# Kernel tuning notes

Hardware: AMD Instinct MI355X
Metric: run time of the kernel (lower is better)

## Reference

```python
import jax, jax.numpy as jnp
import numpy as np
from jax import lax

SCORE_THRESHOLD = 0.01
NMS_THRESHOLD = 0.5
MAX_DETECTIONS = 100
PRE_NMS_TOPK = 512  # fixed-shape candidate pool per class (tf NMS is unbounded; 512 >> max_detections covers it)
NEG_INF = -jnp.inf


def setup_inputs() -> dict:
    key = jax.random.key(0)
    k1, k2, k3, k4, k5 = jax.random.split(key, 5)
    B, N, C = 32, 50000, 10
    # valid (x1,y1,x2,y2) boxes: random top-left + positive width/height
    xy = jax.random.uniform(k1, (B, N, 2), dtype=jnp.float32) * 500.0
    wh = jax.random.uniform(k2, (B, N, 2), dtype=jnp.float32) * 100.0 + 1.0
    boxes = jnp.concatenate([xy, xy + wh], axis=-1)
    classification = jax.random.uniform(k3, (B, N, C), dtype=jnp.float32)
    rotation = jax.random.normal(k4, (B, N, 3), dtype=jnp.float32)
    translation = jax.random.normal(k5, (B, N, 3), dtype=jnp.float32)
    return {"boxes": boxes, "classification": classification,
            "rotation": rotation, "translation": translation}


def _iou_matrix(b):  # b: (K,4) in (x1,y1,x2,y2)
    x1, y1, x2, y2 = b[:, 0], b[:, 1], b[:, 2], b[:, 3]
    area = (x2 - x1) * (y2 - y1)  # (K,)
    ix1 = jnp.maximum(x1[:, None], x1[None, :])
    iy1 = jnp.maximum(y1[:, None], y1[None, :])
    ix2 = jnp.minimum(x2[:, None], x2[None, :])
    iy2 = jnp.minimum(y2[:, None], y2[None, :])
    inter = jnp.maximum(ix2 - ix1, 0.0) * jnp.maximum(iy2 - iy1, 0.0)
    union = area[:, None] + area[None, :] - inter
    return jnp.where(union > 0.0, inter / union, 0.0)  # (K,K)


def _greedy_nms_keep(iou, valid):
    # iou: (K,K) for boxes already sorted by descending score; valid: (K,) bool
    K = iou.shape[0]
    def body(suppressed, xs):
        iou_row, valid_i, i = xs
        keep_i = valid_i & jnp.logical_not(suppressed[i])
        suppressed = jnp.where(keep_i, suppressed | (iou_row > NMS_THRESHOLD), suppressed)
        return suppressed, keep_i
    _, keep = lax.scan(body, jnp.zeros((K,), bool), (iou, valid, jnp.arange(K)))
    return keep


def _per_class(scores, boxes_i):
    # scores: (N,), boxes_i: (N,4) -> kept candidate scores (K,) (-inf where dropped) and anchor idx (K,)
    sc = jnp.where(scores > SCORE_THRESHOLD, scores, NEG_INF)
    vals, idx = lax.top_k(sc, PRE_NMS_TOPK)          # sorted desc
    valid = vals > SCORE_THRESHOLD                    # also false for -inf pads
    iou = _iou_matrix(boxes_i[idx])
    keep = _greedy_nms_keep(iou, valid)
    keep = keep & (jnp.cumsum(keep.astype(jnp.int32)) <= MAX_DETECTIONS)
    return jnp.where(keep, vals, NEG_INF), idx


def _per_image(boxes_i, cls_i, rot_i, trans_i):
    # boxes_i (N,4), cls_i (N,C), rot_i (N,3), trans_i (N,3)
    C = cls_i.shape[1]
    sc_ck, idx_ck = jax.vmap(_per_class, in_axes=(1, None))(cls_i, boxes_i)  # (C,K)
    labels_ck = jnp.broadcast_to(jnp.arange(C, dtype=jnp.int32)[:, None], sc_ck.shape)
    sc_flat = sc_ck.reshape(-1)
    idx_flat = idx_ck.reshape(-1)
    lab_flat = labels_ck.reshape(-1)
    top_scores, sel = lax.top_k(sc_flat, MAX_DETECTIONS)   # global top-k across classes
    sel_idx = idx_flat[sel]
    sel_lab = lab_flat[sel]
    valid = jnp.isfinite(top_scores)
    out_boxes = jnp.where(valid[:, None], boxes_i[sel_idx], -1.0)
    out_scores = jnp.where(valid, top_scores, -1.0)
    out_labels = jnp.where(valid, sel_lab, -1).astype(jnp.int32)
    out_rot = jnp.where(valid[:, None], rot_i[sel_idx], -1.0)
    out_trans = jnp.where(valid[:, None], trans_i[sel_idx], -1.0)
    return out_boxes, out_scores, out_labels, out_rot, out_trans


def reference(boxes, classification, rotation, translation):
    return jax.vmap(_per_image)(boxes, classification, rotation, translation)
```

## Files before the change

### kernel.cpp

```cpp
#include <hip/hip_runtime.h>
#include <math.h>

typedef unsigned int u32;
typedef unsigned long long u64;
typedef unsigned short u16;

constexpr int NB   = 32;
constexpr int NN   = 50000;
constexpr int NC   = 10;
constexpr int KK   = 512;
constexpr int MAXD = 100;
constexpr int CAP  = 2048;
constexpr int LCAP = 192;

constexpr int OFF_BOX = 0;
constexpr int OFF_SC  = NB * MAXD * 4;
constexpr int OFF_LB  = OFF_SC + NB * MAXD;
constexpr int OFF_RT  = OFF_LB + NB * MAXD;
constexpr int OFF_TR  = OFF_RT + NB * MAXD * 3;

__device__ __forceinline__ u32 ord_f32(float s) {
  u32 u = __float_as_uint(s);
  return (u & 0x80000000u) ? ~u : (u | 0x80000000u);
}
__device__ __forceinline__ float unord_f32(u32 o) {
  u32 u = (o & 0x80000000u) ? (o & 0x7FFFFFFFu) : ~o;
  return __uint_as_float(u);
}
__device__ __forceinline__ u64 make_key(float s, u32 i) {
  float sp = (s > 0.01f) ? s : -INFINITY;
  return ((u64)ord_f32(sp) << 32) | (u64)(u32)(~i);
}
__device__ __forceinline__ u32 bin8(float x) {
  if (!(x > 0.01f)) return 0;
  u32 q = (u32)(x * 65536.0f);
  q = q > 65535u ? 65535u : q;
  return q >> 8;
}

__global__ __launch_bounds__(512) void init_kernel(u32* __restrict__ ghist,
                                                   u32* __restrict__ gcnt) {
  const int i = blockIdx.x * 512 + threadIdx.x;
  if (i < NB * NC * 256) ghist[i] = 0;
  if (i < NB * NC) gcnt[i] = 0;
}

__global__ __launch_bounds__(512) void hist_kernel(
    const float* __restrict__ cls, u32* __restrict__ ghist) {
  const int blk = blockIdx.x;
  const int b = blk / 10, seg = blk % 10;
  const float* src = cls + (size_t)b * NN * NC + (size_t)seg * 50000;
  __shared__ u32 chist[NC * 256];
  const int t = threadIdx.x;
  for (int i = t; i < NC * 256; i += 512) chist[i] = 0;
  __syncthreads();
  for (int q = t; q < 12500; q += 512) {
    float4 v = ((const float4*)src)[q];
    float arr[4] = {v.x, v.y, v.z, v.w};
#pragma unroll
    for (int k = 0; k < 4; ++k) {
      int e = q * 4 + k;
      int c = e % 10;
      atomicAdd(&chist[c * 256 + bin8(arr[k])], 1u);
    }
  }
  __syncthreads();
  for (int i = t; i < NC * 256; i += 512) {
    u32 v = chist[i];
    if (v) atomicAdd(&ghist[(size_t)(b * NC + (i >> 8)) * 256 + (i & 255)], v);
  }
}

__global__ __launch_bounds__(64) void cstar_kernel(
    const u32* __restrict__ ghist, u32* __restrict__ cstar) {
  const int bc = blockIdx.x;
  const int lane = threadIdx.x;
  const u32* gh = ghist + (size_t)bc * 256;
  u32 h[4], csum = 0;
#pragma unroll
  for (int k = 0; k < 4; ++k) { h[k] = gh[lane * 4 + k]; csum += h[k]; }
  u32 incl = csum;
#pragma unroll
  for (int s = 1; s < 64; s <<= 1) {
    u32 o = __shfl_down(incl, s, 64);
    if (lane + s < 64) incl += o;
  }
  u32 run = incl - csum;
  int dloc = -1;
#pragma unroll
  for (int k = 3; k >= 0; --k) {
    int bin = lane * 4 + k;
    if (bin >= 1 && run < (u32)KK && run + h[k] >= (u32)KK) dloc = bin;
    run += h[k];
  }
  u64 m = __ballot(dloc >= 0);
  int d = 1;
  if (m) d = __shfl(dloc, (int)__builtin_ctzll(m), 64);
  if (lane == 0) cstar[bc] = (u32)d;
}

__global__ __launch_bounds__(512) void gather_kernel(
    const float* __restrict__ cls, const u32* __restrict__ cstar,
    u64* __restrict__ glist, u32* __restrict__ gcnt) {
  const int blk = blockIdx.x;
  const int b = blk / 25, ch = blk % 25;
  const float* src = cls + (size_t)b * NN * NC + (size_t)ch * 20000;
  __shared__ u32 cs[NC];
  __shared__ u32 lcnt[NC];
  __shared__ u32 lbase[NC];
  __shared__ u64 lbuf[NC][LCAP];
  const int t = threadIdx.x;
  if (t < NC) { cs[t] = cstar[b * NC + t]; lcnt[t] = 0; }
  __syncthreads();
  for (int q = t; q < 5000; q += 512) {
    float4 v = ((const float4*)src)[q];
    float arr[4] = {v.x, v.y, v.z, v.w};
#pragma unroll
    for (int k = 0; k < 4; ++k) {
      int e = q * 4 + k;
      int c = e % 10;
      float x = arr[k];
      if (bin8(x) >= cs[c]) {
        u32 idx = (u32)((ch * 20000 + e) / 10);
        u32 p = atomicAdd(&lcnt[c], 1u);
        if (p < (u32)LCAP) {
          lbuf[c][p] = make_key(x, idx);
        } else {
          u32 g = atomicAdd(&gcnt[b * NC + c], 1u);
          if (g < (u32)CAP) glist[(size_t)(b * NC + c) * CAP + g] = make_key(x, idx);
        }
      }
    }
  }
  __syncthreads();
  if (t < NC) {
    u32 n = min(lcnt[t], (u32)LCAP);
    lbase[t] = atomicAdd(&gcnt[b * NC + t], n);
  }
  __syncthreads();
  for (int c = 0; c < NC; ++c) {
    u32 n = min(lcnt[c], (u32)LCAP);
    u32 base = lbase[c];
    for (u32 i = t; i < n; i += 512) {
      u32 p = base + i;
      if (p < (u32)CAP) glist[(size_t)(b * NC + c) * CAP + p] = lbuf[c][i];
    }
  }
}

__global__ __launch_bounds__(512) void selnms_kernel(
    const u64* __restrict__ glist, const u32* __restrict__ gcnt,
    const float* __restrict__ boxes, int* __restrict__ tidx,
    float* __restrict__ ksc) {
  const int bc = blockIdx.x;
  const int b = bc / NC;
  __shared__ __align__(16) u64 cand[CAP];
  __shared__ u64 sel[KK];
  __shared__ float4 bx4[KK];
  __shared__ float ars[KK];
  __shared__ u64 kmask[8];
  __shared__ int s_cnt;
  const int t = threadIdx.x;
  const int lane = t & 63, wv = t >> 6;

  if (t == 0) s_cnt = (int)gcnt[bc];
  sel[t] = make_key(-INFINITY, 0);
  __syncthreads();
  const int M = min(s_cnt, CAP);
  for (int i = t; i < M; i += 512) cand[i] = glist[(size_t)bc * CAP + i];
  __syncthreads();
  for (int i = t; i < M; i += 512) {
    const u64 key = cand[i];
    int rank = 0;
    for (int j = 0; j < M; ++j) rank += (cand[j] > key) ? 1 : 0;
    if (rank < KK) sel[rank] = key;
  }
  __syncthreads();

  const u64 myk = sel[t];
  const int myidx = (int)(~(u32)myk);
  tidx[bc * KK + t] = myidx;
  const float4 bx = *(const float4*)(boxes + ((size_t)b * NN + myidx) * 4);
  bx4[t] = bx;
  ars[t] = (bx.z - bx.x) * (bx.w - bx.y);
  __syncthreads();

  if (wv == 0) {
    float jx1[8], jy1[8], jx2[8], jy2[8], jar[8];
    u64 vw_[8], sup[8], kw[8];
#pragma unroll
    for (int q = 0; q < 8; ++q) {
      const int j = q * 64 + lane;
      float4 bb = bx4[j];
      jx1[q] = bb.x; jy1[q] = bb.y; jx2[q] = bb.z; jy2[q] = bb.w;
      jar[q] = ars[j];
      float sc = unord_f32((u32)(sel[j] >> 32));
      vw_[q] = __ballot(sc > 0.01f);
      sup[q] = 0;
      kw[q] = 0;
    }
    const double C = 0x1.000001p-1;
    int count = 0;
    bool done = false;
#pragma unroll
    for (int w = 0; w < 8; ++w) {
      if (!done) {
        u64 av = vw_[w] & ~sup[w];
        while (av) {
          const int bbit = (int)__builtin_ctzll(av);
          kw[w] |= 1ull << bbit;
          if (++count == MAXD) { done = true; break; }
          const float bix1 = __shfl(jx1[w], bbit, 64);
          const float biy1 = __shfl(jy1[w], bbit, 64);
          const float bix2 = __shfl(jx2[w], bbit, 64);
          const float biy2 = __shfl(jy2[w], bbit, 64);
          const float bia  = __shfl(jar[w], bbit, 64);
#pragma unroll
          for (int q = 0; q < 8; ++q) {
            if (q >= w) {
              float ix1 = fmaxf(bix1, jx1[q]);
              float iy1 = fmaxf(biy1, jy1[q]);
              float ix2 = fminf(bix2, jx2[q]);
              float iy2 = fminf(biy2, jy2[q]);
              float iw = fmaxf(ix2 - ix1, 0.0f);
              float ih = fmaxf(iy2 - iy1, 0.0f);
              float inter = iw * ih;
              float uni = bia + jar[q] - inter;
              bool s = (uni > 0.0f) && (fma(-C, (double)uni, (double)inter) > 0.0);
              sup[q] |= __ballot(s);
            }
          }
          const u64 mask_gt = (bbit == 63) ? 0ull : (~0ull << (bbit + 1));
          av = vw_[w] & ~sup[w] & mask_gt;
        }
      }
    }
    if (lane < 8) {
      u64 word = kw[0];
#pragma unroll
      for (int q = 1; q < 8; ++q) word = (lane == q) ? kw[q] : word;
      kmask[lane] = word;
    }
  }
  __syncthreads();
  {
    float sc = unord_f32((u32)(myk >> 32));
    bool keep = (kmask[wv] >> lane) & 1ull;
    ksc[bc * KK + t] = keep ? sc : -INFINITY;
  }
}

__global__ __launch_bounds__(512) void final_kernel(
    const float* __restrict__ boxes, const float* __restrict__ rot,
    const float* __restrict__ trans, const int* __restrict__ tidx,
    const float* __restrict__ ksc, float* __restrict__ out) {
  const int b = blockIdx.x;
  __shared__ u64 ck[1024];
  __shared__ int cnt;
  const int t = threadIdx.x;
  if (t == 0) cnt = 0;
  __syncthreads();
  for (int j = t; j < NC * KK; j += 512) {
    float s = ksc[b * NC * KK + j];
    if (s != -INFINITY) {
      int p = atomicAdd(&cnt, 1);
      if (p < 1024) ck[p] = ((u64)ord_f32(s) << 32) | (u64)(u32)(~(u32)j);
    }
  }
  __syncthreads();
  const int n = min(cnt, 1024);
  int npow = 128;
  while (npow < n) npow <<= 1;
  for (int i = n + t; i < npow; i += 512) ck[i] = 0;
  __syncthreads();
  for (int k = 2; k <= npow; k <<= 1) {
    for (int j = k >> 1; j > 0; j >>= 1) {
      for (int i = t; i < npow; i += 512) {
        int ixj = i ^ j;
        if (ixj > i) {
          u64 x = ck[i], y = ck[ixj];
          if (((i & k) == 0) ? (x < y) : (x > y)) { ck[i] = y; ck[ixj] = x; }
        }
      }
      __syncthreads();
    }
  }

  if (t < MAXD) {
    float b0 = -1.f, b1 = -1.f, b2 = -1.f, b3 = -1.f;
    float os = -1.f, ol = -1.f;
    float r0 = -1.f, r1 = -1.f, r2 = -1.f;
    float t0 = -1.f, t1 = -1.f, t2 = -1.f;
    if (t < n) {
      u64 k = ck[t];
      int j = (int)(~(u32)k);
      int c = j >> 9, slot = j & (KK - 1);
      int idx = tidx[(b * NC + c) * KK + slot];
      os = unord_f32((u32)(k >> 32));
      ol = (float)c;
      const float4 bx = *(const float4*)(boxes + ((size_t)b * NN + idx) * 4);
      b0 = bx.x; b1 = bx.y; b2 = bx.z; b3 = bx.w;
      const float* rp = rot + ((size_t)b * NN + idx) * 3;
      r0 = rp[0]; r1 = rp[1]; r2 = rp[2];
      const float* tp = trans + ((size_t)b * NN + idx) * 3;
      t0 = tp[0]; t1 = tp[1]; t2 = tp[2];
    }
    const int o = b * MAXD + t;
    out[OFF_BOX + (size_t)o * 4 + 0] = b0;
    out[OFF_BOX + (size_t)o * 4 + 1] = b1;
    out[OFF_BOX + (size_t)o * 4 + 2] = b2;
    out[OFF_BOX + (size_t)o * 4 + 3] = b3;
    out[OFF_SC + o] = os;
    out[OFF_LB + o] = ol;
    out[OFF_RT + (size_t)o * 3 + 0] = r0;
    out[OFF_RT + (size_t)o * 3 + 1] = r1;
    out[OFF_RT + (size_t)o * 3 + 2] = r2;
    out[OFF_TR + (size_t)o * 3 + 0] = t0;
    out[OFF_TR + (size_t)o * 3 + 1] = t1;
    out[OFF_TR + (size_t)o * 3 + 2] = t2;
  }
}

extern "C" void kernel_launch(void* const* d_in, const int* in_sizes, int n_in,
                              void* d_out, int out_size, void* d_ws, size_t ws_size,
                              hipStream_t stream) {
  const float* boxes = (const float*)d_in[0];
  const float* cls   = (const float*)d_in[1];
  const float* rot   = (const float*)d_in[2];
  const float* trans = (const float*)d_in[3];
  float* out = (float*)d_out;

  u64* glist = (u64*)d_ws;
  int* tidx  = (int*)(glist + (size_t)NB * NC * CAP);
  float* ksc = (float*)(tidx + NB * NC * KK);
  u32* ghist = (u32*)(ksc + NB * NC * KK);
  u32* gcnt  = ghist + NB * NC * 256;
  u32* cstar = gcnt + NB * NC;

  init_kernel<<<161, 512, 0, stream>>>(ghist, gcnt);
  hist_kernel<<<NB * 10, 512, 0, stream>>>(cls, ghist);
  cstar_kernel<<<NB * NC, 64, 0, stream>>>(ghist, cstar);
  gather_kernel<<<NB * 25, 512, 0, stream>>>(cls, cstar, glist, gcnt);
  selnms_kernel<<<NB * NC, 512, 0, stream>>>(glist, gcnt, boxes, tidx, ksc);
  final_kernel<<<NB, 512, 0, stream>>>(boxes, rot, trans, tidx, ksc, out);
}
```

Measured before the change: 137.6 us.

## Halve selnms block size, read pivot box from LDS, rank-select final top-k

Measured after the change: 153.3 us. 11.4% more time.

```diff
diff --git a/kernel.cpp b/kernel.cpp
--- a/kernel.cpp
+++ b/kernel.cpp
@@ -148,7 +148,7 @@
   }
 }
 
-__global__ __launch_bounds__(512) void selnms_kernel(
+__global__ __launch_bounds__(256) void selnms_kernel(
     const u64* __restrict__ glist, const u32* __restrict__ gcnt,
     const float* __restrict__ boxes, int* __restrict__ tidx,
     float* __restrict__ ksc) {
@@ -165,11 +165,12 @@
 
   if (t == 0) s_cnt = (int)gcnt[bc];
   sel[t] = make_key(-INFINITY, 0);
+  sel[t + 256] = make_key(-INFINITY, 0);
   __syncthreads();
   const int M = min(s_cnt, CAP);
-  for (int i = t; i < M; i += 512) cand[i] = glist[(size_t)bc * CAP + i];
-  __syncthreads();
-  for (int i = t; i < M; i += 512) {
+  for (int i = t; i < M; i += 256) cand[i] = glist[(size_t)bc * CAP + i];
+  __syncthreads();
+  for (int i = t; i < M; i += 256) {
     const u64 key = cand[i];
     int rank = 0;
     for (int j = 0; j < M; ++j) rank += (cand[j] > key) ? 1 : 0;
@@ -177,12 +178,16 @@
   }
   __syncthreads();
 
-  const u64 myk = sel[t];
-  const int myidx = (int)(~(u32)myk);
-  tidx[bc * KK + t] = myidx;
-  const float4 bx = *(const float4*)(boxes + ((size_t)b * NN + myidx) * 4);
-  bx4[t] = bx;
-  ars[t] = (bx.z - bx.x) * (bx.w - bx.y);
+#pragma unroll
+  for (int h = 0; h < 2; ++h) {
+    const int s = h * 256 + t;
+    const u64 k = sel[s];
+    const int idx = (int)(~(u32)k);
+    tidx[bc * KK + s] = idx;
+    const float4 bx = *(const float4*)(boxes + ((size_t)b * NN + idx) * 4);
+    bx4[s] = bx;
+    ars[s] = (bx.z - bx.x) * (bx.w - bx.y);
+  }
   __syncthreads();
 
   if (wv == 0) {
@@ -208,24 +213,22 @@
         u64 av = vw_[w] & ~sup[w];
         while (av) {
           const int bbit = (int)__builtin_ctzll(av);
+          const int i = w * 64 + bbit;
           kw[w] |= 1ull << bbit;
           if (++count == MAXD) { done = true; break; }
-          const float bix1 = __shfl(jx1[w], bbit, 64);
-          const float biy1 = __shfl(jy1[w], bbit, 64);
-          const float bix2 = __shfl(jx2[w], bbit, 64);
-          const float biy2 = __shfl(jy2[w], bbit, 64);
-          const float bia  = __shfl(jar[w], bbit, 64);
+          const float4 bi = bx4[i];
+          const float ai = ars[i];
 #pragma unroll
           for (int q = 0; q < 8; ++q) {
             if (q >= w) {
-              float ix1 = fmaxf(bix1, jx1[q]);
-              float iy1 = fmaxf(biy1, jy1[q]);
-              float ix2 = fminf(bix2, jx2[q]);
-              float iy2 = fminf(biy2, jy2[q]);
+              float ix1 = fmaxf(bi.x, jx1[q]);
+              float iy1 = fmaxf(bi.y, jy1[q]);
+              float ix2 = fminf(bi.z, jx2[q]);
+              float iy2 = fminf(bi.w, jy2[q]);
               float iw = fmaxf(ix2 - ix1, 0.0f);
               float ih = fmaxf(iy2 - iy1, 0.0f);
               float inter = iw * ih;
-              float uni = bia + jar[q] - inter;
+              float uni = ai + jar[q] - inter;
               bool s = (uni > 0.0f) && (fma(-C, (double)uni, (double)inter) > 0.0);
               sup[q] |= __ballot(s);
             }
@@ -243,10 +246,12 @@
     }
   }
   __syncthreads();
-  {
-    float sc = unord_f32((u32)(myk >> 32));
-    bool keep = (kmask[wv] >> lane) & 1ull;
-    ksc[bc * KK + t] = keep ? sc : -INFINITY;
+#pragma unroll
+  for (int h = 0; h < 2; ++h) {
+    const int s = h * 256 + t;
+    float sc = unord_f32((u32)(sel[s] >> 32));
+    bool keep = (kmask[s >> 6] >> (s & 63)) & 1ull;
+    ksc[bc * KK + s] = keep ? sc : -INFINITY;
   }
 }
 
@@ -256,9 +261,11 @@
     const float* __restrict__ ksc, float* __restrict__ out) {
   const int b = blockIdx.x;
   __shared__ u64 ck[1024];
+  __shared__ u64 top[MAXD];
   __shared__ int cnt;
   const int t = threadIdx.x;
   if (t == 0) cnt = 0;
+  if (t < MAXD) top[t] = make_key(-INFINITY, 0);
   __syncthreads();
   for (int j = t; j < NC * KK; j += 512) {
     float s = ksc[b * NC * KK + j];
@@ -269,34 +276,26 @@
   }
   __syncthreads();
   const int n = min(cnt, 1024);
-  int npow = 128;
-  while (npow < n) npow <<= 1;
-  for (int i = n + t; i < npow; i += 512) ck[i] = 0;
-  __syncthreads();
-  for (int k = 2; k <= npow; k <<= 1) {
-    for (int j = k >> 1; j > 0; j >>= 1) {
-      for (int i = t; i < npow; i += 512) {
-        int ixj = i ^ j;
-        if (ixj > i) {
-          u64 x = ck[i], y = ck[ixj];
-          if (((i & k) == 0) ? (x < y) : (x > y)) { ck[i] = y; ck[ixj] = x; }
-        }
-      }
-      __syncthreads();
-    }
-  }
+  for (int i = t; i < n; i += 512) {
+    const u64 key = ck[i];
+    int rank = 0;
+    for (int j = 0; j < n; ++j) rank += (ck[j] > key) ? 1 : 0;
+    if (rank < MAXD) top[rank] = key;
+  }
+  __syncthreads();
 
   if (t < MAXD) {
     float b0 = -1.f, b1 = -1.f, b2 = -1.f, b3 = -1.f;
     float os = -1.f, ol = -1.f;
     float r0 = -1.f, r1 = -1.f, r2 = -1.f;
     float t0 = -1.f, t1 = -1.f, t2 = -1.f;
-    if (t < n) {
-      u64 k = ck[t];
+    const u64 k = top[t];
+    const float sc = unord_f32((u32)(k >> 32));
+    if (sc != -INFINITY) {
       int j = (int)(~(u32)k);
       int c = j >> 9, slot = j & (KK - 1);
       int idx = tidx[(b * NC + c) * KK + slot];
-      os = unord_f32((u32)(k >> 32));
+      os = sc;
       ol = (float)c;
       const float4 bx = *(const float4*)(boxes + ((size_t)b * NN + idx) * 4);
       b0 = bx.x; b1 = bx.y; b2 = bx.z; b3 = bx.w;
@@ -341,6 +340,6 @@
   hist_kernel<<<NB * 10, 512, 0, stream>>>(cls, ghist);
   cstar_kernel<<<NB * NC, 64, 0, stream>>>(ghist, cstar);
   gather_kernel<<<NB * 25, 512, 0, stream>>>(cls, cstar, glist, gcnt);
-  selnms_kernel<<<NB * NC, 512, 0, stream>>>(glist, gcnt, boxes, tidx, ksc);
+  selnms_kernel<<<NB * NC, 256, 0, stream>>>(glist, gcnt, boxes, tidx, ksc);
   final_kernel<<<NB, 512, 0, stream>>>(boxes, rot, trans, tidx, ksc, out);
 }
```
